# Performance work log

Hardware: AMD Instinct MI355X
Metric: run time of the kernel (lower is better)

Reference implementation:

```python
import jax, jax.numpy as jnp
import numpy as np

IN_F = 4096
OUT_F = 4096
R_BLOCKS = 4
D = IN_F // R_BLOCKS          # 1024 block size
NUM_TASKS = 5
POOL = 5
EPS0 = 1e-05
SEQ = 4096


def setup_inputs() -> dict:
    key = jax.random.key(0)
    k1, k2, k3, k4 = jax.random.split(key, 4)
    return {
        "input": jax.random.normal(k1, (1, SEQ, IN_F), jnp.float32),
        "lora_route": jax.random.normal(k2, (NUM_TASKS, IN_F, POOL), jnp.float32) * 0.02,
        "lora_down": jax.random.normal(k3, (NUM_TASKS, R_BLOCKS, D, D), jnp.float32) * 0.01,
        "W": jax.random.normal(k4, (OUT_F, IN_F), jnp.float32) * 0.02,
        "task_id": 5,
    }


def _block_diag(Q):
    # Q: [r, d, d] -> [r*d, r*d] block-diagonal
    r, d, _ = Q.shape
    out = jnp.zeros((r * d, r * d), Q.dtype)
    for i in range(r):
        out = out.at[i * d:(i + 1) * d, i * d:(i + 1) * d].set(Q[i])
    return out


def reference(input, lora_route, lora_down, W, task_id):
    # eval-mode forward of OFTInjectedLinear (block_share=False, is_coft=True)
    n_tasks, in_f, pool = lora_route.shape
    r, d = lora_down.shape[1], lora_down.shape[2]
    # project_batch: eps = (eps0 * d * d) / sqrt(r)
    eps = jnp.asarray(EPS0 * d * d, input.dtype) / jnp.sqrt(jnp.asarray(r, input.dtype))

    route = lora_route[task_id - 1][None]                     # [1, in, pool]
    input_mean = jnp.mean(input, axis=1, keepdims=True)       # [1, 1, in]
    omegas = jax.nn.softmax(jnp.matmul(input_mean, route), axis=2)  # [1, 1, pool]
    omegas_mean = jnp.mean(omegas, axis=(0, 1))[:task_id]     # [task_id]
    k = min(task_id, 2)
    _, I_idx = jax.lax.top_k(omegas_mean, k)                  # selected tasks

    eye_d = jnp.eye(d, dtype=input.dtype)
    delta = jnp.eye(in_f, dtype=input.dtype)
    for i in range(k):                                        # k is a small static int
        j = I_idx[i]
        R = jnp.take(lora_down, j, axis=0)                    # [r, d, d]
        # COFT projection toward the ZERO matrix (source uses torch.zeros for I)
        nrm = jnp.sqrt(jnp.sum(R * R, axis=(1, 2), keepdims=True))  # per-block fro norm
        Rp = jnp.where(nrm <= eps, R, eps * R / jnp.maximum(nrm, 1e-12))
        # batched Cayley: Q = (I - skew) (I + skew)^{-1}
        skew = 0.5 * (Rp - jnp.swapaxes(Rp, 1, 2))
        Q = jnp.matmul(eye_d - skew, jnp.linalg.inv(eye_d + skew))  # [r, d, d]
        bd = _block_diag(Q)                                   # [in, in]
        omega_j = omegas[0, 0, j]                             # scalar (B==1)
        delta = delta * (omega_j * bd)                        # ELEMENTWISE, as in source

    filt = jnp.matmul(delta, W.T)                             # [in, out]
    return jnp.matmul(input, filt)                            # [1, S, out]
```

## Files before the change

kernel.cpp:

```cpp
#include <hip/hip_runtime.h>
#include <stdint.h>


typedef __bf16 bf16;
typedef __bf16 bf16x4 __attribute__((ext_vector_type(4)));
typedef __bf16 bf16x8 __attribute__((ext_vector_type(8)));
typedef float  f32x4  __attribute__((ext_vector_type(4)));

#define AS1 __attribute__((address_space(1)))
#define AS3 __attribute__((address_space(3)))

constexpr size_t OFF_INBF = 0;
constexpr size_t OFF_WV   = OFF_INBF + (size_t)4096 * 4096 * 2;
constexpr size_t OFF_MEAN = OFF_WV + (size_t)4096 * 4096 * 2;
constexpr size_t OFF_INFO = OFF_MEAN + 4096 * 4;
constexpr size_t OFF_V    = OFF_INFO + 64;
constexpr size_t TP_ELEMS = (size_t)16 * 8192;

__global__ void mean_cvt(const float4* __restrict__ in4, float* __restrict__ meansum,
                         bf16* __restrict__ ob) {
    const int t  = threadIdx.x;
    const int f4 = blockIdx.x * 256 + t;
    const int s0 = blockIdx.y * 32;
    float sx = 0.f, sy = 0.f, sz = 0.f, sw = 0.f;
    for (int s = s0; s < s0 + 32; ++s) {
        float4 vx = in4[(size_t)s * 1024 + f4];
        sx += vx.x; sy += vx.y; sz += vx.z; sw += vx.w;
        bf16x4 bv;
        bv[0] = (bf16)vx.x; bv[1] = (bf16)vx.y; bv[2] = (bf16)vx.z; bv[3] = (bf16)vx.w;
        *(bf16x4*)&ob[(size_t)s * 4096 + f4 * 4] = bv;
    }
    atomicAdd(&meansum[f4 * 4 + 0], sx);
    atomicAdd(&meansum[f4 * 4 + 1], sy);
    atomicAdd(&meansum[f4 * 4 + 2], sz);
    atomicAdd(&meansum[f4 * 4 + 3], sw);
}

__global__ void omega_kernel(const float* __restrict__ meansum, const float* __restrict__ lora_route,
                             const int* __restrict__ task_id_p, int* __restrict__ info_i,
                             float* __restrict__ info_f) {
    __shared__ float red[256];
    __shared__ float logits[5];
    const int t = threadIdx.x;
    const int tid = task_id_p[0];
    const float* route = lora_route + (size_t)(tid - 1) * 4096 * 5;
    float acc[5] = {0.f, 0.f, 0.f, 0.f, 0.f};
    for (int f = t; f < 4096; f += 256) {
        float m = meansum[f] * (1.0f / 4096.0f);
#pragma unroll
        for (int p = 0; p < 5; ++p) acc[p] += m * route[f * 5 + p];
    }
    for (int p = 0; p < 5; ++p) {
        red[t] = acc[p];
        __syncthreads();
        for (int s = 128; s > 0; s >>= 1) {
            if (t < s) red[t] += red[t + s];
            __syncthreads();
        }
        if (t == 0) logits[p] = red[0];
        __syncthreads();
    }
    if (t == 0) {
        float mx = logits[0];
        for (int p = 1; p < 5; ++p) mx = fmaxf(mx, logits[p]);
        float e[5], se = 0.f;
        for (int p = 0; p < 5; ++p) { e[p] = expf(logits[p] - mx); se += e[p]; }
        float om[5];
        for (int p = 0; p < 5; ++p) om[p] = e[p] / se;
        const int n = tid < 5 ? tid : 5;
        int j1 = 0;
        for (int p = 1; p < n; ++p) if (om[p] > om[j1]) j1 = p;
        int j2 = -1;
        for (int p = 0; p < n; ++p) if (p != j1 && (j2 < 0 || om[p] > om[j2])) j2 = p;
        const int k = tid < 2 ? tid : 2;
        info_i[0] = j1;
        info_i[1] = (k > 1) ? j2 : j1;
        info_i[2] = k;
        float c = om[j1];
        if (k > 1) c *= om[j2];
        info_f[3] = c;
    }
}

__global__ void diag_kernel(const float* __restrict__ lora_down, const int* __restrict__ info_i,
                            float* __restrict__ TP, float* __restrict__ NP) {
    const int bid = blockIdx.x;
    const int ts = bid >> 10;
    const int rb = (bid >> 8) & 3;
    const int a  = (bid >> 4) & 15;
    const int b  = bid & 15;
    const int k = info_i[2];
    if (ts >= k) return;
    const int j = info_i[ts];
    const float* R = lora_down + ((size_t)(j * 4 + rb) << 20);
    __shared__ float X[64][65];
    __shared__ float Y[64][65];
    __shared__ float wsum[4];
    const int t = threadIdx.x;
    const int i = t >> 2, g = t & 3;
    const int a64 = a * 64, b64 = b * 64;
    float nacc = 0.f;
#pragma unroll
    for (int qq = 0; qq < 4; ++qq) {
        const int fi = qq * 256 + t;
        const int row = fi >> 4, c4 = fi & 15;
        float4 vx = *(const float4*)&R[(size_t)(a64 + row) * 1024 + b64 + c4 * 4];
        X[row][c4 * 4 + 0] = vx.x; X[row][c4 * 4 + 1] = vx.y;
        X[row][c4 * 4 + 2] = vx.z; X[row][c4 * 4 + 3] = vx.w;
        nacc += vx.x * vx.x + vx.y * vx.y + vx.z * vx.z + vx.w * vx.w;
        float4 vy = *(const float4*)&R[(size_t)(b64 + row) * 1024 + a64 + c4 * 4];
        Y[row][c4 * 4 + 0] = vy.x; Y[row][c4 * 4 + 1] = vy.y;
        Y[row][c4 * 4 + 2] = vy.z; Y[row][c4 * 4 + 3] = vy.w;
    }
    __syncthreads();
    float tacc = 0.f;
#pragma unroll
    for (int s = 0; s < 16; ++s) {
        float d = X[i][g * 16 + s] - Y[g * 16 + s][i];
        tacc += d * d;
    }
    tacc += __shfl_xor(tacc, 1);
    tacc += __shfl_xor(tacc, 2);
    if (g == 0) TP[b * 8192 + ((ts * 4 + rb) << 10) + a64 + i] = tacc;
    for (int off = 32; off > 0; off >>= 1) nacc += __shfl_down(nacc, off);
    if ((t & 63) == 0) wsum[t >> 6] = nacc;
    __syncthreads();
    if (t == 0) NP[(ts * 4 + rb) * 256 + a * 16 + b] = wsum[0] + wsum[1] + wsum[2] + wsum[3];
}

__global__ void vbuild(const float* __restrict__ TP, const float* __restrict__ NP,
                       const int* __restrict__ info_i, const float* __restrict__ info_f,
                       float* __restrict__ v) {
    __shared__ float red[256];
    __shared__ float snrm[8];
    const int t = threadIdx.x;
    for (int g = 0; g < 8; ++g) {
        red[t] = NP[g * 256 + t];
        __syncthreads();
        for (int s = 128; s > 0; s >>= 1) {
            if (t < s) red[t] += red[t + s];
            __syncthreads();
        }
        if (t == 0) snrm[g] = red[0];
        __syncthreads();
    }
    const int i = blockIdx.x * 256 + t;
    const int k = info_i[2];
    const float c = info_f[3];
    const int rb = i >> 10, di = i & 1023;
    const float eps = 1e-5f * 1024.0f * 1024.0f / 2.0f;
    float q = c;
    for (int ts = 0; ts < k; ++ts) {
        float tt = 0.f;
#pragma unroll
        for (int bb = 0; bb < 16; ++bb) tt += TP[bb * 8192 + ((ts * 4 + rb) << 10) + di];
        float nrm = sqrtf(snrm[ts * 4 + rb]);
        float scale = (nrm <= eps) ? 1.0f : eps / fmaxf(nrm, 1e-12f);
        q *= 1.0f - 0.5f * scale * scale * tt;
    }
    v[i] = q;
}

__global__ void scaleW(const float4* __restrict__ W4, const float* __restrict__ v,
                       bf16* __restrict__ Wv) {
    const size_t stride = (size_t)gridDim.x * blockDim.x;
    for (size_t i = (size_t)blockIdx.x * blockDim.x + threadIdx.x; i < (size_t)4096 * 1024; i += stride) {
        float4 w = W4[i];
        const float* vp = &v[(i & 1023) << 2];
        bf16x4 o;
        o[0] = (bf16)(w.x * vp[0]);
        o[1] = (bf16)(w.y * vp[1]);
        o[2] = (bf16)(w.z * vp[2]);
        o[3] = (bf16)(w.w * vp[3]);
        *(bf16x4*)&Wv[i << 2] = o;
    }
}

__device__ __forceinline__ void gload_lds16(const bf16* g, bf16* lds) {
    __builtin_amdgcn_global_load_lds((const AS1 void*)g, (AS3 void*)lds, 16, 0, 0);
}

__global__ __launch_bounds__(512, 2) void gemm256(const bf16* __restrict__ A,
                                                  const bf16* __restrict__ B,
                                                  float* __restrict__ C) {
    __shared__ bf16 lds[65536];
    const int t = threadIdx.x;
    const int w = t >> 6, l = t & 63;
    const int bid = blockIdx.x;
    const int swz = ((bid & 7) << 5) | (bid >> 3);
    const int bm = swz >> 4, bn = swz & 15;
    const int wm = w >> 2, wn = w & 3;
    const int rl = l & 15, q = l >> 4;
    const int xm = (l & 7) << 4;

    const int srow = (w << 4) + (l >> 3);
    const int scol = ((l & 7) ^ (l >> 3)) << 3;
    const bf16* pA = A + (size_t)((bm << 8) + srow) * 4096 + scol;
    const bf16* pB = B + (size_t)((bn << 8) + srow) * 4096 + scol;

#define STG(dstE, srcP, h, kt) do {                                                          \
        gload_lds16((srcP) + (size_t)((h) * 128) * 4096 + (size_t)(kt) * 64,                 \
                    (bf16*)&lds[(dstE) + (h) * 8192 + w * 1024]);                            \
        gload_lds16((srcP) + (size_t)((h) * 128 + 8) * 4096 + (size_t)(kt) * 64,             \
                    (bf16*)&lds[(dstE) + (h) * 8192 + w * 1024 + 512]);                      \
    } while (0)

    const int aB = (((wm << 7) + rl) << 6);
    const int bB = 16384 + (((wn << 6) + rl) << 6);
    const int c0 = (((q << 4) + 0) ^ xm) >> 1;
    const int c1 = (((q << 4) + 64) ^ xm) >> 1;

    f32x4 acc[8][4] = {};

    STG(0, pA, 0, 0); STG(0, pA, 1, 0);
    STG(16384, pB, 0, 0); STG(16384, pB, 1, 0);
    STG(32768, pA, 0, 1); STG(32768, pA, 1, 1);

    for (int kt = 0; kt < 64; ++kt) {
        const int bufE = (kt & 1) << 15;
        const int nb = bufE ^ 32768;
        if (kt < 63) asm volatile("s_waitcnt vmcnt(4)" ::: "memory");
        else         asm volatile("s_waitcnt vmcnt(0)" ::: "memory");
        __builtin_amdgcn_s_barrier();
        asm volatile("" ::: "memory");

        bf16x8 a0[8], b0[4], a1[8], b1[4];
#pragma unroll
        for (int m = 0; m < 8; ++m) a0[m] = *(const bf16x8*)&lds[bufE + aB + m * 1024 + c0];
#pragma unroll
        for (int n = 0; n < 4; ++n) b0[n] = *(const bf16x8*)&lds[bufE + bB + n * 1024 + c0];
        if (kt + 1 < 64) STG(nb + 16384, pB, 0, kt + 1);
        __builtin_amdgcn_s_setprio(1);
#pragma unroll
        for (int m = 0; m < 4; ++m)
#pragma unroll
            for (int n = 0; n < 4; ++n)
                acc[m][n] = __builtin_amdgcn_mfma_f32_16x16x32_bf16(a0[m], b0[n], acc[m][n], 0, 0, 0);
        __builtin_amdgcn_s_setprio(0);
        __builtin_amdgcn_s_barrier();

#pragma unroll
        for (int m = 0; m < 8; ++m) a1[m] = *(const bf16x8*)&lds[bufE + aB + m * 1024 + c1];
#pragma unroll
        for (int n = 0; n < 4; ++n) b1[n] = *(const bf16x8*)&lds[bufE + bB + n * 1024 + c1];
        if (kt + 1 < 64) STG(nb + 16384, pB, 1, kt + 1);
        __builtin_amdgcn_s_setprio(1);
#pragma unroll
        for (int m = 4; m < 8; ++m)
#pragma unroll
            for (int n = 0; n < 4; ++n)
                acc[m][n] = __builtin_amdgcn_mfma_f32_16x16x32_bf16(a0[m], b0[n], acc[m][n], 0, 0, 0);
        __builtin_amdgcn_s_setprio(0);
        asm volatile("s_waitcnt lgkmcnt(0)" ::: "memory");
        __builtin_amdgcn_s_barrier();

        if (kt + 2 < 64) STG(bufE, pA, 0, kt + 2);
        __builtin_amdgcn_s_setprio(1);
#pragma unroll
        for (int m = 0; m < 4; ++m)
#pragma unroll
            for (int n = 0; n < 4; ++n)
                acc[m][n] = __builtin_amdgcn_mfma_f32_16x16x32_bf16(a1[m], b1[n], acc[m][n], 0, 0, 0);
        __builtin_amdgcn_s_setprio(0);
        __builtin_amdgcn_s_barrier();

        if (kt + 2 < 64) STG(bufE, pA, 1, kt + 2);
        __builtin_amdgcn_s_setprio(1);
#pragma unroll
        for (int m = 4; m < 8; ++m)
#pragma unroll
            for (int n = 0; n < 4; ++n)
                acc[m][n] = __builtin_amdgcn_mfma_f32_16x16x32_bf16(a1[m], b1[n], acc[m][n], 0, 0, 0);
        __builtin_amdgcn_s_setprio(0);
    }
#undef STG

    const int crow = (bm << 8) + (wm << 7) + (q << 2);
    const int ccol = (bn << 8) + (wn << 6) + rl;
#pragma unroll
    for (int m = 0; m < 8; ++m)
#pragma unroll
        for (int n = 0; n < 4; ++n)
#pragma unroll
            for (int r = 0; r < 4; ++r)
                C[(size_t)(crow + m * 16 + r) * 4096 + ccol + n * 16] = acc[m][n][r];
}

extern "C" void kernel_launch(void* const* d_in, const int* in_sizes, int n_in,
                              void* d_out, int out_size, void* d_ws, size_t ws_size,
                              hipStream_t stream) {
    const float* input      = (const float*)d_in[0];
    const float* lora_route = (const float*)d_in[1];
    const float* lora_down  = (const float*)d_in[2];
    const float* W          = (const float*)d_in[3];
    const int*   task_id    = (const int*)d_in[4];

    char* ws = (char*)d_ws;
    bf16*  inbf    = (bf16*)(ws + OFF_INBF);
    bf16*  Wv      = (bf16*)(ws + OFF_WV);
    float* meansum = (float*)(ws + OFF_MEAN);
    int*   info_i  = (int*)(ws + OFF_INFO);
    float* info_f  = (float*)(ws + OFF_INFO);
    float* v       = (float*)(ws + OFF_V);
    float* TP      = (float*)(ws + OFF_WV);
    float* NP      = TP + TP_ELEMS;
    float* out     = (float*)d_out;

    hipMemsetAsync(meansum, 0, 4096 * 4, stream);

    mean_cvt<<<dim3(4, 128), 256, 0, stream>>>((const float4*)input, meansum, inbf);
    omega_kernel<<<1, 256, 0, stream>>>(meansum, lora_route, task_id, info_i, info_f);
    diag_kernel<<<2048, 256, 0, stream>>>(lora_down, info_i, TP, NP);
    vbuild<<<16, 256, 0, stream>>>(TP, NP, info_i, info_f, v);
    scaleW<<<4096, 256, 0, stream>>>((const float4*)W, v, Wv);
    gemm256<<<256, 512, 0, stream>>>(inbf, Wv, out);
}
```

Before: 202.7 us.

## Software-pipeline LDS fragment loads across k-iterations in bf16 GEMM main loop

Splits the A fragments into low and high halves and reorders the LDS reads so each MFMA phase consumes registers loaded during the previous phase. The first A fragments of the next k-tile are prefetched before the last MFMA phase of the current tile. Both A-tile global-to-LDS stages are issued together, with an extra vmcnt wait. This is meant to hide LDS read latency behind MFMA work, at the cost of more live registers and a changed wait/barrier schedule that could stall or lower occupancy.

```diff
diff --git a/kernel.cpp b/kernel.cpp
--- a/kernel.cpp
+++ b/kernel.cpp
@@ -211,67 +211,83 @@
     const int c1 = (((q << 4) + 64) ^ xm) >> 1;
 
     f32x4 acc[8][4] = {};
+    bf16x8 a0L[4], a0H[4], a1L[4], a1H[4], b0[4], b1[4], a0n[4];
 
     STG(0, pA, 0, 0); STG(0, pA, 1, 0);
     STG(16384, pB, 0, 0); STG(16384, pB, 1, 0);
     STG(32768, pA, 0, 1); STG(32768, pA, 1, 1);
+    asm volatile("s_waitcnt vmcnt(8)" ::: "memory");
+    __builtin_amdgcn_s_barrier();
+    asm volatile("" ::: "memory");
+#pragma unroll
+    for (int m = 0; m < 4; ++m) a0L[m] = *(const bf16x8*)&lds[0 + aB + m * 1024 + c0];
 
     for (int kt = 0; kt < 64; ++kt) {
-        const int bufE = (kt & 1) << 15;
-        const int nb = bufE ^ 32768;
+        const int cur = (kt & 1) << 15;
+        const int nxt = cur ^ 32768;
         if (kt < 63) asm volatile("s_waitcnt vmcnt(4)" ::: "memory");
         else         asm volatile("s_waitcnt vmcnt(0)" ::: "memory");
         __builtin_amdgcn_s_barrier();
         asm volatile("" ::: "memory");
 
-        bf16x8 a0[8], b0[4], a1[8], b1[4];
-#pragma unroll
-        for (int m = 0; m < 8; ++m) a0[m] = *(const bf16x8*)&lds[bufE + aB + m * 1024 + c0];
-#pragma unroll
-        for (int n = 0; n < 4; ++n) b0[n] = *(const bf16x8*)&lds[bufE + bB + n * 1024 + c0];
-        if (kt + 1 < 64) STG(nb + 16384, pB, 0, kt + 1);
+#pragma unroll
+        for (int n = 0; n < 4; ++n) b0[n] = *(const bf16x8*)&lds[cur + bB + n * 1024 + c0];
+#pragma unroll
+        for (int m = 0; m < 4; ++m) a0H[m] = *(const bf16x8*)&lds[cur + aB + (m + 4) * 1024 + c0];
+        if (kt + 1 < 64) STG(nxt + 16384, pB, 0, kt + 1);
         __builtin_amdgcn_s_setprio(1);
 #pragma unroll
         for (int m = 0; m < 4; ++m)
 #pragma unroll
             for (int n = 0; n < 4; ++n)
-                acc[m][n] = __builtin_amdgcn_mfma_f32_16x16x32_bf16(a0[m], b0[n], acc[m][n], 0, 0, 0);
+                acc[m][n] = __builtin_amdgcn_mfma_f32_16x16x32_bf16(a0L[m], b0[n], acc[m][n], 0, 0, 0);
         __builtin_amdgcn_s_setprio(0);
         __builtin_amdgcn_s_barrier();
 
 #pragma unroll
-        for (int m = 0; m < 8; ++m) a1[m] = *(const bf16x8*)&lds[bufE + aB + m * 1024 + c1];
-#pragma unroll
-        for (int n = 0; n < 4; ++n) b1[n] = *(const bf16x8*)&lds[bufE + bB + n * 1024 + c1];
-        if (kt + 1 < 64) STG(nb + 16384, pB, 1, kt + 1);
+        for (int m = 0; m < 4; ++m) a1L[m] = *(const bf16x8*)&lds[cur + aB + m * 1024 + c1];
+#pragma unroll
+        for (int n = 0; n < 4; ++n) b1[n] = *(const bf16x8*)&lds[cur + bB + n * 1024 + c1];
+        if (kt + 1 < 64) STG(nxt + 16384, pB, 1, kt + 1);
         __builtin_amdgcn_s_setprio(1);
 #pragma unroll
-        for (int m = 4; m < 8; ++m)
+        for (int m = 0; m < 4; ++m)
 #pragma unroll
             for (int n = 0; n < 4; ++n)
-                acc[m][n] = __builtin_amdgcn_mfma_f32_16x16x32_bf16(a0[m], b0[n], acc[m][n], 0, 0, 0);
+                acc[m + 4][n] = __builtin_amdgcn_mfma_f32_16x16x32_bf16(a0H[m], b0[n], acc[m + 4][n], 0, 0, 0);
+        __builtin_amdgcn_s_setprio(0);
+        __builtin_amdgcn_s_barrier();
+
+#pragma unroll
+        for (int m = 0; m < 4; ++m) a1H[m] = *(const bf16x8*)&lds[cur + aB + (m + 4) * 1024 + c1];
+        __builtin_amdgcn_s_setprio(1);
+#pragma unroll
+        for (int m = 0; m < 4; ++m)
+#pragma unroll
+            for (int n = 0; n < 4; ++n)
+                acc[m][n] = __builtin_amdgcn_mfma_f32_16x16x32_bf16(a1L[m], b1[n], acc[m][n], 0, 0, 0);
         __builtin_amdgcn_s_setprio(0);
         asm volatile("s_waitcnt lgkmcnt(0)" ::: "memory");
+        if (kt < 63) asm volatile("s_waitcnt vmcnt(4)" ::: "memory");
         __builtin_amdgcn_s_barrier();
-
-        if (kt + 2 < 64) STG(bufE, pA, 0, kt + 2);
+        asm volatile("" ::: "memory");
+
+        if (kt + 2 < 64) { STG(cur, pA, 0, kt + 2); STG(cur, pA, 1, kt + 2); }
+        if (kt + 1 < 64) {
+#pragma unroll
+            for (int m = 0; m < 4; ++m) a0n[m] = *(const bf16x8*)&lds[nxt + aB + m * 1024 + c0];
+        }
         __builtin_amdgcn_s_setprio(1);
 #pragma unroll
         for (int m = 0; m < 4; ++m)
 #pragma unroll
             for (int n = 0; n < 4; ++n)
-                acc[m][n] = __builtin_amdgcn_mfma_f32_16x16x32_bf16(a1[m], b1[n], acc[m][n], 0, 0, 0);
+                acc[m + 4][n] = __builtin_amdgcn_mfma_f32_16x16x32_bf16(a1H[m], b1[n], acc[m + 4][n], 0, 0, 0);
         __builtin_amdgcn_s_setprio(0);
-        __builtin_amdgcn_s_barrier();
-
-        if (kt + 2 < 64) STG(bufE, pA, 1, kt + 2);
-        __builtin_amdgcn_s_setprio(1);
-#pragma unroll
-        for (int m = 4; m < 8; ++m)
-#pragma unroll
-            for (int n = 0; n < 4; ++n)
-                acc[m][n] = __builtin_amdgcn_mfma_f32_16x16x32_bf16(a1[m], b1[n], acc[m][n], 0, 0, 0);
-        __builtin_amdgcn_s_setprio(0);
+        if (kt + 1 < 64) {
+#pragma unroll
+            for (int m = 0; m < 4; ++m) a0L[m] = a0n[m];
+        }
     }
 #undef STG
 
```

New measurement: 201.6 us (median of 4 runs). Within noise of the previous version (-0.5%).
